# Kernel optimization log

Measured on AMD Instinct MI355X. Metric: run time of the kernel, lower is better.

## Reference

```python
import jax, jax.numpy as jnp
import numpy as np

B, P, DIM, H, HKV = 4, 2048, 1024, 16, 8
D = DIM // H  # head_dim = 64


def setup_inputs() -> dict:
    key = jax.random.key(0)
    ks = jax.random.split(key, 5)
    s = lambda fan: 1.0 / np.sqrt(fan)
    return {
        "x": jax.random.normal(ks[0], (B, P, DIM), jnp.float32),
        "Wq": jax.random.normal(ks[1], (DIM, DIM), jnp.float32) * s(DIM),
        "Wk": jax.random.normal(ks[2], (DIM, HKV * D), jnp.float32) * s(DIM),
        "Wv": jax.random.normal(ks[3], (DIM, HKV * D), jnp.float32) * s(DIM),
        "Wp": jax.random.normal(ks[4], (DIM, DIM), jnp.float32) * s(DIM),
        "bp": jnp.zeros((DIM,), jnp.float32),
        "cache": jnp.zeros((HKV,), jnp.float32),  # registered buffer, starts at zero
    }


def _ratios(k, cache):
    # k: [B, HKV, P, D]; torch.norm over dims (2,3) then sum over batch -> [HKV]
    mags = jnp.sqrt((k * k).sum(axis=(2, 3))).sum(axis=0)
    diff = jnp.abs(cache - mags)
    r = jnp.round(diff / diff.sum() * H).astype(jnp.int32)
    # Deterministic repair of rounding so sum(r) == H (original uses random indices)
    r = jax.lax.while_loop(lambda r: r.sum() > H,
                           lambda r: r.at[jnp.argmax(r)].add(-1), r)
    r = jax.lax.while_loop(lambda r: r.sum() < H,
                           lambda r: r.at[jnp.argmin(r)].add(1), r)
    return r


def reference(x, Wq, Wk, Wv, Wp, bp, cache):
    # qkv projections (no bias, per qkv_bias=False)
    q = (x @ Wq).reshape(B, P, H, D).transpose(0, 2, 1, 3) * (D ** -0.5)  # [B,H,P,D]
    k = (x @ Wk).reshape(B, P, HKV, D).transpose(0, 2, 1, 3)              # [B,HKV,P,D]
    v = (x @ Wv).reshape(B, P, HKV, D).transpose(0, 2, 1, 3)

    # dynamic group sizes per kv head (inference path: cache <- magnitudes)
    ratios = jax.lax.stop_gradient(_ratios(k, cache))  # [HKV], sums to H
    # map each query head h to its kv head: group i owns heads [cumsum[i-1], cumsum[i])
    kv_id = jnp.searchsorted(jnp.cumsum(ratios), jnp.arange(H), side='right')

    # gather kv per query head -> identical math to the per-group loop, fully fused
    kf = k[:, kv_id]  # [B,H,P,D]
    vf = v[:, kv_id]
    scores = jnp.einsum('bhqd,bhkd->bhqk', q, kf)   # [B,H,P,P]
    w = jax.nn.softmax(scores, axis=-1)             # attn_drop p=0 -> identity
    out = jnp.einsum('bhqk,bhkd->bhqd', w, vf)
    out = out.transpose(0, 2, 1, 3).reshape(B, P, DIM)
    return out @ Wp + bp  # proj (proj_drop p=0)
```

## Files before the change

kernel.cpp:

```cpp
#include <hip/hip_runtime.h>

typedef __bf16 bf16x8 __attribute__((ext_vector_type(8)));
typedef __bf16 bf16x4 __attribute__((ext_vector_type(4)));
typedef float floatx4 __attribute__((ext_vector_type(4)));

#define BSZ 4
#define SEQ 2048
#define DIM 1024
#define NH 16
#define NKV 8
#define HD 64

#define GLDS16(g, l) __builtin_amdgcn_global_load_lds(                        \
    (const __attribute__((address_space(1))) void*)(g),                       \
    (__attribute__((address_space(3))) void*)(l), 16, 0, 0)

__global__ __launch_bounds__(256) void prep_kernel(
    const float* __restrict__ x,
    const float* __restrict__ Wq, const float* __restrict__ Wk,
    const float* __restrict__ Wv, const float* __restrict__ Wp,
    __bf16* __restrict__ xb, __bf16* __restrict__ Wt, __bf16* __restrict__ Wpt)
{
    __shared__ __bf16 T[64][72];
    const int bid = blockIdx.x;
    const int tid = threadIdx.x;

    if (bid < 2048) {
        size_t i = ((size_t)bid * 256 + tid) * 16;
#pragma unroll
        for (int q = 0; q < 2; ++q) {
            float4 a = *(const float4*)&x[i + q * 8];
            float4 b = *(const float4*)&x[i + q * 8 + 4];
            bf16x8 o;
            o[0] = (__bf16)a.x; o[1] = (__bf16)a.y; o[2] = (__bf16)a.z; o[3] = (__bf16)a.w;
            o[4] = (__bf16)b.x; o[5] = (__bf16)b.y; o[6] = (__bf16)b.z; o[7] = (__bf16)b.w;
            *(bf16x8*)&xb[i + q * 8] = o;
        }
        return;
    }

    const int t  = bid - 2048;
    const int k0 = (t & 15) * 64;
    const int cg = (t >> 4) * 64;

    const float* W; int ldn, cl, orow; __bf16* out;
    if (cg < 1024)      { W = Wq; ldn = 1024; cl = cg;        out = Wt;  orow = cg; }
    else if (cg < 1536) { W = Wk; ldn = 512;  cl = cg - 1024; out = Wt;  orow = cg; }
    else if (cg < 2048) { W = Wv; ldn = 512;  cl = cg - 1536; out = Wt;  orow = cg; }
    else                { W = Wp; ldn = 1024; cl = cg - 2048; out = Wpt; orow = cg - 2048; }

    const int kr = tid >> 2;
    const int cq = (tid & 3) * 16;
#pragma unroll
    for (int j = 0; j < 4; ++j) {
        float4 f = *(const float4*)&W[(size_t)(k0 + kr) * ldn + cl + cq + j * 4];
        T[cq + j * 4 + 0][kr] = (__bf16)f.x;
        T[cq + j * 4 + 1][kr] = (__bf16)f.y;
        T[cq + j * 4 + 2][kr] = (__bf16)f.z;
        T[cq + j * 4 + 3][kr] = (__bf16)f.w;
    }
    __syncthreads();
#pragma unroll
    for (int j = 0; j < 2; ++j) {
        int ch = tid * 2 + j;
        int c = ch >> 3, kc = (ch & 7) * 8;
        *(bf16x8*)&out[(size_t)(orow + c) * 1024 + k0 + kc] = *(bf16x8*)&T[c][kc];
    }
}

__global__ __launch_bounds__(256) void qkv_gemm(
    const __bf16* __restrict__ xb, const __bf16* __restrict__ Wt,
    __bf16* __restrict__ qw, __bf16* __restrict__ kw, __bf16* __restrict__ vw)
{
    __shared__ __align__(16) __bf16 As[128 * 32];
    __shared__ __align__(16) __bf16 Bs[128 * 32];

    const int m0 = blockIdx.y * 128;
    const int c0 = blockIdx.x * 128;

    const int tid  = threadIdx.x;
    const int lane = tid & 63, wv = tid >> 6;
    const int l16  = lane & 15, quad = lane >> 4;
    const int wr = (wv >> 1) * 64, wc = (wv & 1) * 64;

    const int srow = wv * 16 + (lane >> 2);
    const int skc  = (lane & 3) * 8;
    const __bf16* Ag = xb + (size_t)(m0 + srow) * 1024 + skc;
    const __bf16* Bg = Wt + (size_t)(c0 + srow) * 1024 + skc;
    __bf16* lA = As + wv * 512;
    __bf16* lB = Bs + wv * 512;

    floatx4 acc[4][4] = {};

    for (int k0 = 0; k0 < 1024; k0 += 32) {
        GLDS16(Ag + k0,             lA);
        GLDS16(Ag + k0 + 64 * 1024, lA + 2048);
        GLDS16(Bg + k0,             lB);
        GLDS16(Bg + k0 + 64 * 1024, lB + 2048);
        __syncthreads();

        bf16x8 af[4], bfr[4];
#pragma unroll
        for (int t = 0; t < 4; ++t) {
            af[t]  = *(bf16x8*)&As[(wr + t * 16 + l16) * 32 + quad * 8];
            bfr[t] = *(bf16x8*)&Bs[(wc + t * 16 + l16) * 32 + quad * 8];
        }
#pragma unroll
        for (int mt = 0; mt < 4; ++mt)
#pragma unroll
            for (int nt = 0; nt < 4; ++nt)
                acc[mt][nt] = __builtin_amdgcn_mfma_f32_16x16x32_bf16(
                    af[mt], bfr[nt], acc[mt][nt], 0, 0, 0);
        __syncthreads();
    }

#pragma unroll
    for (int mt = 0; mt < 4; ++mt) {
#pragma unroll
        for (int nt = 0; nt < 4; ++nt) {
#pragma unroll
            for (int r = 0; r < 4; ++r) {
                int m = m0 + wr + mt * 16 + quad * 4 + r;
                int c = c0 + wc + nt * 16 + l16;
                int bb = m >> 11, p = m & 2047;
                float val = acc[mt][nt][r];
                if (c < 1024) {
                    int h = c >> 6, d = c & 63;
                    qw[(((size_t)bb * NH + h) * SEQ + p) * HD + d] = (__bf16)(val * 0.125f);
                } else if (c < 1536) {
                    int cc = c - 1024, hh = cc >> 6, d = cc & 63;
                    kw[(((size_t)bb * NKV + hh) * SEQ + p) * HD + d] = (__bf16)val;
                } else {
                    int cc = c - 1536, hh = cc >> 6, d = cc & 63;
                    vw[(((size_t)bb * NKV + hh) * HD + d) * SEQ + p] = (__bf16)val;
                }
            }
        }
    }
}

__global__ __launch_bounds__(256) void ksumsq(const __bf16* __restrict__ kw,
                                              float* __restrict__ partial)
{
    const int blk = blockIdx.x;
    const __bf16* base = kw + (size_t)(blk >> 3) * (SEQ * HD)
                            + (size_t)(blk & 7) * (SEQ * HD / 8);
    const int tid = threadIdx.x;

    float s = 0.f;
#pragma unroll
    for (int i = tid * 8; i < SEQ * HD / 8; i += 256 * 8) {
        bf16x8 vv = *(const bf16x8*)&base[i];
#pragma unroll
        for (int j = 0; j < 8; ++j) { float f = (float)vv[j]; s += f * f; }
    }
#pragma unroll
    for (int off = 1; off < 64; off <<= 1) s += __shfl_xor(s, off, 64);

    __shared__ float red[4];
    if ((tid & 63) == 0) red[tid >> 6] = s;
    __syncthreads();
    if (tid == 0) partial[blk] = red[0] + red[1] + red[2] + red[3];
}

__global__ void ratios_kernel(const float* __restrict__ partial,
                              const float* __restrict__ cache,
                              int* __restrict__ kv_id)
{
    if (threadIdx.x != 0 || blockIdx.x != 0) return;
    float mag[8] = {0.f, 0.f, 0.f, 0.f, 0.f, 0.f, 0.f, 0.f};
    for (int b = 0; b < 4; ++b)
        for (int j = 0; j < 8; ++j) {
            float ss = 0.f;
            for (int sl = 0; sl < 8; ++sl) ss += partial[(b * 8 + j) * 8 + sl];
            mag[j] += sqrtf(ss);
        }
    float diff[8], sum = 0.f;
    for (int j = 0; j < 8; ++j) {
        diff[j] = fabsf(cache[j] - mag[j]);
        sum += diff[j];
    }
    int r[8], s = 0;
    for (int j = 0; j < 8; ++j) {
        r[j] = (int)rintf(diff[j] / sum * 16.0f);
        s += r[j];
    }
    while (s > 16) {
        int jm = 0;
        for (int j = 1; j < 8; ++j) if (r[j] > r[jm]) jm = j;
        r[jm]--; s--;
    }
    while (s < 16) {
        int jm = 0;
        for (int j = 1; j < 8; ++j) if (r[j] < r[jm]) jm = j;
        r[jm]++; s++;
    }
    int cum[8], c = 0;
    for (int j = 0; j < 8; ++j) { c += r[j]; cum[j] = c; }
    for (int h = 0; h < 16; ++h) {
        int j = 0;
        while (j < 7 && cum[j] <= h) j++;
        kv_id[h] = j;
    }
}

__global__ __launch_bounds__(256, 4) void attn_kernel(
    const __bf16* __restrict__ qw, const __bf16* __restrict__ kw,
    const __bf16* __restrict__ vw, const int* __restrict__ kv_id,
    __bf16* __restrict__ attn_out)
{
    __shared__ __align__(16) __bf16 Kt[2][64 * 72];
    __shared__ __align__(16) __bf16 VT[2][64 * 72];

    const int bh = blockIdx.y;
    const int b = bh >> 4, h = bh & 15;
    const int q0 = blockIdx.x * 128;
    const int kv = kv_id[h];

    const __bf16* Kg = kw + ((size_t)(b * NKV + kv) * SEQ) * HD;
    const __bf16* Vg = vw + ((size_t)(b * NKV + kv) * HD) * SEQ;
    const __bf16* Qg = qw + ((size_t)(b * NH + h) * SEQ + q0) * HD;

    const int tid  = threadIdx.x;
    const int lane = tid & 63, wv = tid >> 6;
    const int l16  = lane & 15, quad = lane >> 4;

    bf16x8 qf[2][2];
#pragma unroll
    for (int s = 0; s < 2; ++s) {
        const __bf16* qp = &Qg[(size_t)(32 * wv + 16 * s + l16) * HD];
        qf[s][0] = *(const bf16x8*)&qp[quad * 8];
        qf[s][1] = *(const bf16x8*)&qp[32 + quad * 8];
    }

    float l_acc[2] = {0.f, 0.f};
    floatx4 o[2][4] = {};

    const int row = tid >> 2, cc = (tid & 3) << 4;
    const __bf16* kp = Kg + (size_t)row * HD + cc;
    const __bf16* vp = Vg + (size_t)row * SEQ + cc;

    bf16x8 rk0 = *(const bf16x8*)kp;
    bf16x8 rk1 = *(const bf16x8*)(kp + 8);
    bf16x8 rv0 = *(const bf16x8*)vp;
    bf16x8 rv1 = *(const bf16x8*)(vp + 8);
    {
        __bf16* kd = &Kt[0][row * 72 + cc];
        *(bf16x8*)kd = rk0; *(bf16x8*)(kd + 8) = rk1;
        __bf16* vd = &VT[0][row * 72 + cc];
        *(bf16x8*)vd = rv0; *(bf16x8*)(vd + 8) = rv1;
    }
    __syncthreads();

    for (int kb = 0; kb < 32; ++kb) {
        const int cur = kb & 1;
        const __bf16* Kc = &Kt[cur][0];
        const __bf16* Vc = &VT[cur][0];

        floatx4 sacc[2][4] = {};
        {
            bf16x8 kf[4];
#pragma unroll
            for (int t = 0; t < 4; ++t)
                kf[t] = *(bf16x8*)&Kc[(16 * t + l16) * 72 + quad * 8];
#pragma unroll
            for (int t = 0; t < 4; ++t) {
                sacc[0][t] = __builtin_amdgcn_mfma_f32_16x16x32_bf16(kf[t], qf[0][0], sacc[0][t], 0, 0, 0);
                sacc[1][t] = __builtin_amdgcn_mfma_f32_16x16x32_bf16(kf[t], qf[1][0], sacc[1][t], 0, 0, 0);
            }
#pragma unroll
            for (int t = 0; t < 4; ++t)
                kf[t] = *(bf16x8*)&Kc[(16 * t + l16) * 72 + 32 + quad * 8];
#pragma unroll
            for (int t = 0; t < 4; ++t) {
                sacc[0][t] = __builtin_amdgcn_mfma_f32_16x16x32_bf16(kf[t], qf[0][1], sacc[0][t], 0, 0, 0);
                sacc[1][t] = __builtin_amdgcn_mfma_f32_16x16x32_bf16(kf[t], qf[1][1], sacc[1][t], 0, 0, 0);
            }
        }

        if (kb < 31) {
            const __bf16* kn = kp + (size_t)(kb + 1) * (64 * HD);
            const __bf16* vn = vp + (kb + 1) * 64;
            rk0 = *(const bf16x8*)kn;
            rk1 = *(const bf16x8*)(kn + 8);
            rv0 = *(const bf16x8*)vn;
            rv1 = *(const bf16x8*)(vn + 8);
        }

        bf16x8 a0s[2], a1s[2];
#pragma unroll
        for (int s = 0; s < 2; ++s) {
            bf16x8 a0, a1;
#pragma unroll
            for (int r = 0; r < 4; ++r) {
                float e0 = __expf(sacc[s][0][r] - 10.f); l_acc[s] += e0;
                float e1 = __expf(sacc[s][1][r] - 10.f); l_acc[s] += e1;
                float e2 = __expf(sacc[s][2][r] - 10.f); l_acc[s] += e2;
                float e3 = __expf(sacc[s][3][r] - 10.f); l_acc[s] += e3;
                a0[r] = (__bf16)e0; a0[4 + r] = (__bf16)e1;
                a1[r] = (__bf16)e2; a1[4 + r] = (__bf16)e3;
            }
            a0s[s] = a0; a1s[s] = a1;
        }

#pragma unroll
        for (int dt = 0; dt < 4; ++dt) {
            const __bf16* vrow = &Vc[(16 * dt + l16) * 72 + 4 * quad];
            bf16x4 lo0 = *(const bf16x4*)vrow;
            bf16x4 hi0 = *(const bf16x4*)(vrow + 16);
            bf16x8 vb0 = __builtin_shufflevector(lo0, hi0, 0, 1, 2, 3, 4, 5, 6, 7);
            o[0][dt] = __builtin_amdgcn_mfma_f32_16x16x32_bf16(a0s[0], vb0, o[0][dt], 0, 0, 0);
            o[1][dt] = __builtin_amdgcn_mfma_f32_16x16x32_bf16(a0s[1], vb0, o[1][dt], 0, 0, 0);
            bf16x4 lo1 = *(const bf16x4*)(vrow + 32);
            bf16x4 hi1 = *(const bf16x4*)(vrow + 48);
            bf16x8 vb1 = __builtin_shufflevector(lo1, hi1, 0, 1, 2, 3, 4, 5, 6, 7);
            o[0][dt] = __builtin_amdgcn_mfma_f32_16x16x32_bf16(a1s[0], vb1, o[0][dt], 0, 0, 0);
            o[1][dt] = __builtin_amdgcn_mfma_f32_16x16x32_bf16(a1s[1], vb1, o[1][dt], 0, 0, 0);
        }

        if (kb < 31) {
            __bf16* kd = &Kt[cur ^ 1][row * 72 + cc];
            *(bf16x8*)kd = rk0; *(bf16x8*)(kd + 8) = rk1;
            __bf16* vd = &VT[cur ^ 1][row * 72 + cc];
            *(bf16x8*)vd = rv0; *(bf16x8*)(vd + 8) = rv1;
        }
        __syncthreads();
    }

#pragma unroll
    for (int s = 0; s < 2; ++s) {
        float l = l_acc[s];
        l += __shfl_xor(l, 16, 64);
        l += __shfl_xor(l, 32, 64);
#pragma unroll
        for (int r = 0; r < 4; ++r) {
            float lr = __shfl(l, quad * 4 + r, 64);
            float inv = 1.f / lr;
            int p_ = q0 + 32 * wv + 16 * s + quad * 4 + r;
#pragma unroll
            for (int dt = 0; dt < 4; ++dt) {
                int d = 16 * dt + l16;
                attn_out[(((size_t)b * SEQ + p_) * NH + h) * HD + d] = (__bf16)(o[s][dt][r] * inv);
            }
        }
    }
}

__global__ __launch_bounds__(256) void proj_gemm(
    const __bf16* __restrict__ A, const __bf16* __restrict__ Wpt,
    const float* __restrict__ bp, float* __restrict__ out)
{
    __shared__ __align__(16) __bf16 As[128 * 32];
    __shared__ __align__(16) __bf16 Bs[128 * 32];

    const int m0 = blockIdx.y * 128, c0 = blockIdx.x * 128;
    const int tid = threadIdx.x, lane = tid & 63, wv = tid >> 6;
    const int l16 = lane & 15, quad = lane >> 4;
    const int wr = (wv >> 1) * 64, wc = (wv & 1) * 64;

    const int srow = wv * 16 + (lane >> 2);
    const int skc  = (lane & 3) * 8;
    const __bf16* Ag = A   + (size_t)(m0 + srow) * 1024 + skc;
    const __bf16* Bg = Wpt + (size_t)(c0 + srow) * 1024 + skc;
    __bf16* lA = As + wv * 512;
    __bf16* lB = Bs + wv * 512;

    floatx4 acc[4][4] = {};

    for (int k0 = 0; k0 < 1024; k0 += 32) {
        GLDS16(Ag + k0,             lA);
        GLDS16(Ag + k0 + 64 * 1024, lA + 2048);
        GLDS16(Bg + k0,             lB);
        GLDS16(Bg + k0 + 64 * 1024, lB + 2048);
        __syncthreads();

        bf16x8 af[4], bfr[4];
#pragma unroll
        for (int t = 0; t < 4; ++t) {
            af[t]  = *(bf16x8*)&As[(wr + t * 16 + l16) * 32 + quad * 8];
            bfr[t] = *(bf16x8*)&Bs[(wc + t * 16 + l16) * 32 + quad * 8];
        }
#pragma unroll
        for (int mt = 0; mt < 4; ++mt)
#pragma unroll
            for (int nt = 0; nt < 4; ++nt)
                acc[mt][nt] = __builtin_amdgcn_mfma_f32_16x16x32_bf16(
                    af[mt], bfr[nt], acc[mt][nt], 0, 0, 0);
        __syncthreads();
    }

#pragma unroll
    for (int nt = 0; nt < 4; ++nt) {
        int c = c0 + wc + nt * 16 + l16;
        float bias = bp[c];
#pragma unroll
        for (int mt = 0; mt < 4; ++mt)
#pragma unroll
            for (int r = 0; r < 4; ++r) {
                int m = m0 + wr + mt * 16 + quad * 4 + r;
                out[(size_t)m * 1024 + c] = acc[mt][nt][r] + bias;
            }
    }
}

extern "C" void kernel_launch(void* const* d_in, const int* in_sizes, int n_in,
                              void* d_out, int out_size, void* d_ws, size_t ws_size,
                              hipStream_t stream)
{
    const float* x     = (const float*)d_in[0];
    const float* Wq    = (const float*)d_in[1];
    const float* Wk    = (const float*)d_in[2];
    const float* Wv    = (const float*)d_in[3];
    const float* Wp    = (const float*)d_in[4];
    const float* bp    = (const float*)d_in[5];
    const float* cache = (const float*)d_in[6];
    float* outp = (float*)d_out;

    __bf16* ws = (__bf16*)d_ws;
    __bf16* qw  = ws;
    __bf16* kw  = qw + (size_t)BSZ * NH * SEQ * HD;
    __bf16* vw  = kw + (size_t)BSZ * NKV * SEQ * HD;
    __bf16* at  = vw + (size_t)BSZ * NKV * SEQ * HD;
    __bf16* xb  = at + (size_t)BSZ * NH * SEQ * HD;
    __bf16* Wt  = xb + (size_t)BSZ * SEQ * DIM;
    __bf16* Wpt = Wt + (size_t)2048 * 1024;
    float* partial = (float*)(Wpt + (size_t)1024 * 1024);
    int*   kv_id   = (int*)(partial + 256);

    prep_kernel<<<2816, 256, 0, stream>>>(x, Wq, Wk, Wv, Wp, xb, Wt, Wpt);
    qkv_gemm<<<dim3(16, 64), 256, 0, stream>>>(xb, Wt, qw, kw, vw);
    ksumsq<<<256, 256, 0, stream>>>(kw, partial);
    ratios_kernel<<<1, 64, 0, stream>>>(partial, cache, kv_id);
    attn_kernel<<<dim3(16, 64), 256, 0, stream>>>(qw, kw, vw, kv_id, at);
    proj_gemm<<<dim3(8, 64), 256, 0, stream>>>(at, Wpt, bp, outp);
}
```

Before: 296.9 us.

## Double-buffer swizzled GEMMs, fuse K norm into QKV epilogue, prioritize attention MFMA

Both GEMMs move to 512-thread blocks with 256x128 tiles and K-step 64. LDS is double-buffered with XOR swizzling so the next stage's global-to-LDS loads overlap the current MFMAs with one barrier per step. The K sum-of-squares is computed in the QKV epilogue and atomically added to a 32-entry buffer, which removes the separate ksumsq kernel and its reread of K; the buffer is zeroed in prep_kernel. The attention MFMA sections are wrapped in s_setprio. The trade-offs are nondeterministic float atomics, norms taken from fp32 values rather than bf16-rounded ones, and heavier LDS use per block, which may lower occupancy.

```diff
diff --git a/kernel.cpp b/kernel.cpp
--- a/kernel.cpp
+++ b/kernel.cpp
@@ -19,13 +19,15 @@
     const float* __restrict__ x,
     const float* __restrict__ Wq, const float* __restrict__ Wk,
     const float* __restrict__ Wv, const float* __restrict__ Wp,
-    __bf16* __restrict__ xb, __bf16* __restrict__ Wt, __bf16* __restrict__ Wpt)
+    __bf16* __restrict__ xb, __bf16* __restrict__ Wt, __bf16* __restrict__ Wpt,
+    float* __restrict__ partial)
 {
     __shared__ __bf16 T[64][72];
     const int bid = blockIdx.x;
     const int tid = threadIdx.x;
 
     if (bid < 2048) {
+        if (bid == 0 && tid < 32) partial[tid] = 0.f;
         size_t i = ((size_t)bid * 256 + tid) * 16;
 #pragma unroll
         for (int q = 0; q < 2; ++q) {
@@ -68,52 +70,71 @@
     }
 }
 
-__global__ __launch_bounds__(256) void qkv_gemm(
+#define STAGE(bufi, kof)                                                      \
+    {                                                                         \
+        _Pragma("unroll") for (int i = 0; i < 4; ++i)                         \
+            GLDS16(Ag + (kof) + i * 64 * 1024, &As[bufi][i * 4096 + w512]);   \
+        _Pragma("unroll") for (int i = 0; i < 2; ++i)                         \
+            GLDS16(Bg + (kof) + i * 64 * 1024, &Bs[bufi][i * 4096 + w512]);   \
+    }
+
+__global__ __launch_bounds__(512) void qkv_gemm(
     const __bf16* __restrict__ xb, const __bf16* __restrict__ Wt,
-    __bf16* __restrict__ qw, __bf16* __restrict__ kw, __bf16* __restrict__ vw)
-{
-    __shared__ __align__(16) __bf16 As[128 * 32];
-    __shared__ __align__(16) __bf16 Bs[128 * 32];
-
-    const int m0 = blockIdx.y * 128;
+    __bf16* __restrict__ qw, __bf16* __restrict__ kw, __bf16* __restrict__ vw,
+    float* __restrict__ partial)
+{
+    __shared__ __align__(16) __bf16 As[2][256 * 64];
+    __shared__ __align__(16) __bf16 Bs[2][128 * 64];
+
+    const int m0 = blockIdx.y * 256;
     const int c0 = blockIdx.x * 128;
 
     const int tid  = threadIdx.x;
     const int lane = tid & 63, wv = tid >> 6;
     const int l16  = lane & 15, quad = lane >> 4;
     const int wr = (wv >> 1) * 64, wc = (wv & 1) * 64;
-
-    const int srow = wv * 16 + (lane >> 2);
-    const int skc  = (lane & 3) * 8;
-    const __bf16* Ag = xb + (size_t)(m0 + srow) * 1024 + skc;
-    const __bf16* Bg = Wt + (size_t)(c0 + srow) * 1024 + skc;
-    __bf16* lA = As + wv * 512;
-    __bf16* lB = Bs + wv * 512;
+    const int w512 = wv * 512;
+
+    const int srow = wv * 8 + (lane >> 3);
+    const int scol = ((lane & 7) ^ (lane >> 3)) * 8;
+    const __bf16* Ag = xb + (size_t)(m0 + srow) * 1024 + scol;
+    const __bf16* Bg = Wt + (size_t)(c0 + srow) * 1024 + scol;
+
+    const int sw0 = ((quad)     ^ (l16 & 7)) * 8;
+    const int sw1 = ((4 + quad) ^ (l16 & 7)) * 8;
 
     floatx4 acc[4][4] = {};
 
-    for (int k0 = 0; k0 < 1024; k0 += 32) {
-        GLDS16(Ag + k0,             lA);
-        GLDS16(Ag + k0 + 64 * 1024, lA + 2048);
-        GLDS16(Bg + k0,             lB);
-        GLDS16(Bg + k0 + 64 * 1024, lB + 2048);
+    STAGE(0, 0);
+    __syncthreads();
+
+    for (int t = 0; t < 16; ++t) {
+        const int cur = t & 1;
+        if (t < 15) STAGE(cur ^ 1, (t + 1) * 64);
+
+        bf16x8 af[4][2], bfr[4][2];
+#pragma unroll
+        for (int tt = 0; tt < 4; ++tt) {
+            const int ar = (wr + tt * 16 + l16) * 64;
+            af[tt][0] = *(bf16x8*)&As[cur][ar + sw0];
+            af[tt][1] = *(bf16x8*)&As[cur][ar + sw1];
+            const int br = (wc + tt * 16 + l16) * 64;
+            bfr[tt][0] = *(bf16x8*)&Bs[cur][br + sw0];
+            bfr[tt][1] = *(bf16x8*)&Bs[cur][br + sw1];
+        }
+#pragma unroll
+        for (int mt = 0; mt < 4; ++mt)
+#pragma unroll
+            for (int nt = 0; nt < 4; ++nt) {
+                acc[mt][nt] = __builtin_amdgcn_mfma_f32_16x16x32_bf16(
+                    af[mt][0], bfr[nt][0], acc[mt][nt], 0, 0, 0);
+                acc[mt][nt] = __builtin_amdgcn_mfma_f32_16x16x32_bf16(
+                    af[mt][1], bfr[nt][1], acc[mt][nt], 0, 0, 0);
+            }
         __syncthreads();
-
-        bf16x8 af[4], bfr[4];
-#pragma unroll
-        for (int t = 0; t < 4; ++t) {
-            af[t]  = *(bf16x8*)&As[(wr + t * 16 + l16) * 32 + quad * 8];
-            bfr[t] = *(bf16x8*)&Bs[(wc + t * 16 + l16) * 32 + quad * 8];
-        }
-#pragma unroll
-        for (int mt = 0; mt < 4; ++mt)
-#pragma unroll
-            for (int nt = 0; nt < 4; ++nt)
-                acc[mt][nt] = __builtin_amdgcn_mfma_f32_16x16x32_bf16(
-                    af[mt], bfr[nt], acc[mt][nt], 0, 0, 0);
-        __syncthreads();
-    }
-
+    }
+
+    float ss = 0.f;
 #pragma unroll
     for (int mt = 0; mt < 4; ++mt) {
 #pragma unroll
@@ -130,6 +151,7 @@
                 } else if (c < 1536) {
                     int cc = c - 1024, hh = cc >> 6, d = cc & 63;
                     kw[(((size_t)bb * NKV + hh) * SEQ + p) * HD + d] = (__bf16)val;
+                    ss += val * val;
                 } else {
                     int cc = c - 1536, hh = cc >> 6, d = cc & 63;
                     vw[(((size_t)bb * NKV + hh) * HD + d) * SEQ + p] = (__bf16)val;
@@ -137,30 +159,16 @@
             }
         }
     }
-}
-
-__global__ __launch_bounds__(256) void ksumsq(const __bf16* __restrict__ kw,
-                                              float* __restrict__ partial)
-{
-    const int blk = blockIdx.x;
-    const __bf16* base = kw + (size_t)(blk >> 3) * (SEQ * HD)
-                            + (size_t)(blk & 7) * (SEQ * HD / 8);
-    const int tid = threadIdx.x;
-
-    float s = 0.f;
-#pragma unroll
-    for (int i = tid * 8; i < SEQ * HD / 8; i += 256 * 8) {
-        bf16x8 vv = *(const bf16x8*)&base[i];
-#pragma unroll
-        for (int j = 0; j < 8; ++j) { float f = (float)vv[j]; s += f * f; }
-    }
-#pragma unroll
-    for (int off = 1; off < 64; off <<= 1) s += __shfl_xor(s, off, 64);
-
-    __shared__ float red[4];
-    if ((tid & 63) == 0) red[tid >> 6] = s;
-    __syncthreads();
-    if (tid == 0) partial[blk] = red[0] + red[1] + red[2] + red[3];
+
+    if (c0 >= 1024 && c0 < 1536) {
+#pragma unroll
+        for (int off = 1; off < 64; off <<= 1) ss += __shfl_xor(ss, off, 64);
+        if (lane == 0) {
+            int bb = m0 >> 11;
+            int hh = (c0 - 1024 + wc) >> 6;
+            atomicAdd(&partial[bb * 8 + hh], ss);
+        }
+    }
 }
 
 __global__ void ratios_kernel(const float* __restrict__ partial,
@@ -170,11 +178,7 @@
     if (threadIdx.x != 0 || blockIdx.x != 0) return;
     float mag[8] = {0.f, 0.f, 0.f, 0.f, 0.f, 0.f, 0.f, 0.f};
     for (int b = 0; b < 4; ++b)
-        for (int j = 0; j < 8; ++j) {
-            float ss = 0.f;
-            for (int sl = 0; sl < 8; ++sl) ss += partial[(b * 8 + j) * 8 + sl];
-            mag[j] += sqrtf(ss);
-        }
+        for (int j = 0; j < 8; ++j) mag[j] += sqrtf(partial[b * 8 + j]);
     float diff[8], sum = 0.f;
     for (int j = 0; j < 8; ++j) {
         diff[j] = fabsf(cache[j] - mag[j]);
@@ -263,19 +267,23 @@
 #pragma unroll
             for (int t = 0; t < 4; ++t)
                 kf[t] = *(bf16x8*)&Kc[(16 * t + l16) * 72 + quad * 8];
+            __builtin_amdgcn_s_setprio(1);
 #pragma unroll
             for (int t = 0; t < 4; ++t) {
                 sacc[0][t] = __builtin_amdgcn_mfma_f32_16x16x32_bf16(kf[t], qf[0][0], sacc[0][t], 0, 0, 0);
                 sacc[1][t] = __builtin_amdgcn_mfma_f32_16x16x32_bf16(kf[t], qf[1][0], sacc[1][t], 0, 0, 0);
             }
+            __builtin_amdgcn_s_setprio(0);
 #pragma unroll
             for (int t = 0; t < 4; ++t)
                 kf[t] = *(bf16x8*)&Kc[(16 * t + l16) * 72 + 32 + quad * 8];
+            __builtin_amdgcn_s_setprio(1);
 #pragma unroll
             for (int t = 0; t < 4; ++t) {
                 sacc[0][t] = __builtin_amdgcn_mfma_f32_16x16x32_bf16(kf[t], qf[0][1], sacc[0][t], 0, 0, 0);
                 sacc[1][t] = __builtin_amdgcn_mfma_f32_16x16x32_bf16(kf[t], qf[1][1], sacc[1][t], 0, 0, 0);
             }
+            __builtin_amdgcn_s_setprio(0);
         }
 
         if (kb < 31) {
@@ -303,6 +311,7 @@
             a0s[s] = a0; a1s[s] = a1;
         }
 
+        __builtin_amdgcn_s_setprio(1);
 #pragma unroll
         for (int dt = 0; dt < 4; ++dt) {
             const __bf16* vrow = &Vc[(16 * dt + l16) * 72 + 4 * quad];
@@ -317,6 +326,7 @@
             o[0][dt] = __builtin_amdgcn_mfma_f32_16x16x32_bf16(a1s[0], vb1, o[0][dt], 0, 0, 0);
             o[1][dt] = __builtin_amdgcn_mfma_f32_16x16x32_bf16(a1s[1], vb1, o[1][dt], 0, 0, 0);
         }
+        __builtin_amdgcn_s_setprio(0);
 
         if (kb < 31) {
             __bf16* kd = &Kt[cur ^ 1][row * 72 + cc];
@@ -346,46 +356,58 @@
     }
 }
 
-__global__ __launch_bounds__(256) void proj_gemm(
+__global__ __launch_bounds__(512) void proj_gemm(
     const __bf16* __restrict__ A, const __bf16* __restrict__ Wpt,
     const float* __restrict__ bp, float* __restrict__ out)
 {
-    __shared__ __align__(16) __bf16 As[128 * 32];
-    __shared__ __align__(16) __bf16 Bs[128 * 32];
-
-    const int m0 = blockIdx.y * 128, c0 = blockIdx.x * 128;
-    const int tid = threadIdx.x, lane = tid & 63, wv = tid >> 6;
-    const int l16 = lane & 15, quad = lane >> 4;
+    __shared__ __align__(16) __bf16 As[2][256 * 64];
+    __shared__ __align__(16) __bf16 Bs[2][128 * 64];
+
+    const int m0 = blockIdx.y * 256;
+    const int c0 = blockIdx.x * 128;
+
+    const int tid  = threadIdx.x;
+    const int lane = tid & 63, wv = tid >> 6;
+    const int l16  = lane & 15, quad = lane >> 4;
     const int wr = (wv >> 1) * 64, wc = (wv & 1) * 64;
-
-    const int srow = wv * 16 + (lane >> 2);
-    const int skc  = (lane & 3) * 8;
-    const __bf16* Ag = A   + (size_t)(m0 + srow) * 1024 + skc;
-    const __bf16* Bg = Wpt + (size_t)(c0 + srow) * 1024 + skc;
-    __bf16* lA = As + wv * 512;
-    __bf16* lB = Bs + wv * 512;
+    const int w512 = wv * 512;
+
+    const int srow = wv * 8 + (lane >> 3);
+    const int scol = ((lane & 7) ^ (lane >> 3)) * 8;
+    const __bf16* Ag = A   + (size_t)(m0 + srow) * 1024 + scol;
+    const __bf16* Bg = Wpt + (size_t)(c0 + srow) * 1024 + scol;
+
+    const int sw0 = ((quad)     ^ (l16 & 7)) * 8;
+    const int sw1 = ((4 + quad) ^ (l16 & 7)) * 8;
 
     floatx4 acc[4][4] = {};
 
-    for (int k0 = 0; k0 < 1024; k0 += 32) {
-        GLDS16(Ag + k0,             lA);
-        GLDS16(Ag + k0 + 64 * 1024, lA + 2048);
-        GLDS16(Bg + k0,             lB);
-        GLDS16(Bg + k0 + 64 * 1024, lB + 2048);
-        __syncthreads();
-
-        bf16x8 af[4], bfr[4];
-#pragma unroll
-        for (int t = 0; t < 4; ++t) {
-            af[t]  = *(bf16x8*)&As[(wr + t * 16 + l16) * 32 + quad * 8];
-            bfr[t] = *(bf16x8*)&Bs[(wc + t * 16 + l16) * 32 + quad * 8];
+    STAGE(0, 0);
+    __syncthreads();
+
+    for (int t = 0; t < 16; ++t) {
+        const int cur = t & 1;
+        if (t < 15) STAGE(cur ^ 1, (t + 1) * 64);
+
+        bf16x8 af[4][2], bfr[4][2];
+#pragma unroll
+        for (int tt = 0; tt < 4; ++tt) {
+            const int ar = (wr + tt * 16 + l16) * 64;
+            af[tt][0] = *(bf16x8*)&As[cur][ar + sw0];
+            af[tt][1] = *(bf16x8*)&As[cur][ar + sw1];
+            const int br = (wc + tt * 16 + l16) * 64;
+            bfr[tt][0] = *(bf16x8*)&Bs[cur][br + sw0];
+            bfr[tt][1] = *(bf16x8*)&Bs[cur][br + sw1];
         }
 #pragma unroll
         for (int mt = 0; mt < 4; ++mt)
 #pragma unroll
-            for (int nt = 0; nt < 4; ++nt)
+            for (int nt = 0; nt < 4; ++nt) {
                 acc[mt][nt] = __builtin_amdgcn_mfma_f32_16x16x32_bf16(
-                    af[mt], bfr[nt], acc[mt][nt], 0, 0, 0);
+                    af[mt][0], bfr[nt][0], acc[mt][nt], 0, 0, 0);
+                acc[mt][nt] = __builtin_amdgcn_mfma_f32_16x16x32_bf16(
+                    af[mt][1], bfr[nt][1], acc[mt][nt], 0, 0, 0);
+            }
         __syncthreads();
     }
 
@@ -425,12 +447,11 @@
     __bf16* Wt  = xb + (size_t)BSZ * SEQ * DIM;
     __bf16* Wpt = Wt + (size_t)2048 * 1024;
     float* partial = (float*)(Wpt + (size_t)1024 * 1024);
-    int*   kv_id   = (int*)(partial + 256);
-
-    prep_kernel<<<2816, 256, 0, stream>>>(x, Wq, Wk, Wv, Wp, xb, Wt, Wpt);
-    qkv_gemm<<<dim3(16, 64), 256, 0, stream>>>(xb, Wt, qw, kw, vw);
-    ksumsq<<<256, 256, 0, stream>>>(kw, partial);
+    int*   kv_id   = (int*)(partial + 32);
+
+    prep_kernel<<<2816, 256, 0, stream>>>(x, Wq, Wk, Wv, Wp, xb, Wt, Wpt, partial);
+    qkv_gemm<<<dim3(16, 32), 512, 0, stream>>>(xb, Wt, qw, kw, vw, partial);
     ratios_kernel<<<1, 64, 0, stream>>>(partial, cache, kv_id);
     attn_kernel<<<dim3(16, 64), 256, 0, stream>>>(qw, kw, vw, kv_id, at);
-    proj_gemm<<<dim3(8, 64), 256, 0, stream>>>(at, Wpt, bp, outp);
-}
+    proj_gemm<<<dim3(8, 32), 512, 0, stream>>>(at, Wpt, bp, outp);
+}
```

After: 330.3 us. 1.11x slower.
